# Kernel tuning notes

Hardware: AMD Instinct MI355X
Metric: run time of the kernel (lower is better)

## Reference

```python
import jax, jax.numpy as jnp
import numpy as np

N_NODES = 100_000
N_EDGES = 1_200_000
IN_C, HID_C, OUT_C, K = 64, 64, 32, 3


def setup_inputs() -> dict:
    key = jax.random.key(0)
    ks = jax.random.split(key, 8)
    x = jax.random.normal(ks[0], (N_NODES, IN_C), dtype=jnp.float32)
    edge_index = jax.random.randint(ks[1], (2, N_EDGES), 0, N_NODES, dtype=jnp.int64)
    # ChebConv parameters: weight [K, in, out], bias [out] (Glorot-ish scale)
    W1 = jax.random.normal(ks[2], (K, IN_C, HID_C), dtype=jnp.float32) / np.sqrt(IN_C)
    b1 = jnp.zeros((HID_C,), dtype=jnp.float32)
    W2 = jax.random.normal(ks[3], (K, HID_C, OUT_C), dtype=jnp.float32) / np.sqrt(HID_C)
    b2 = jnp.zeros((OUT_C,), dtype=jnp.float32)
    return {"x": x, "edge_index": edge_index, "W1": W1, "b1": b1, "W2": W2, "b2": b2}


def _cheb_conv(x, row, col, norm_w, W, b):
    # Scaled Laplacian with lambda_max=2 (PyG default): L_hat = -D^{-1/2} A D^{-1/2}
    def prop(t):  # L_hat @ t, via edge gather + segment-sum scatter
        msg = norm_w[:, None] * t[col]            # [E, C]
        return -jax.ops.segment_sum(msg, row, num_segments=N_NODES)

    Tx0 = x
    out = Tx0 @ W[0]
    Tx1 = prop(x)
    out = out + Tx1 @ W[1]
    for k in range(2, W.shape[0]):
        Tx2 = 2.0 * prop(Tx1) - Tx0          # Chebyshev recurrence
        out = out + Tx2 @ W[k]
        Tx0, Tx1 = Tx1, Tx2
    return out + b


def reference(x, edge_index, W1, b1, W2, b2):
    row, col = edge_index[0], edge_index[1]
    deg = jax.ops.segment_sum(jnp.ones((row.shape[0],), x.dtype), row,
                              num_segments=N_NODES)
    deg_inv_sqrt = jnp.where(deg > 0, jax.lax.rsqrt(jnp.maximum(deg, 1.0)), 0.0)
    norm_w = deg_inv_sqrt[row] * deg_inv_sqrt[col]   # symmetric normalization

    h = jax.nn.relu(_cheb_conv(x, row, col, norm_w, W1, b1))
    # dropout omitted (eval mode / training=False)
    return _cheb_conv(h, row, col, norm_w, W2, b2)
```

## Files before the change

### kernel.cpp

```cpp
#include <hip/hip_runtime.h>
#include <hip/hip_fp16.h>

#define N_NODES_C 100000
#define N_EDGES_C 1200000
#define NBUK ((N_NODES_C + 255) >> 8)
#define CHUNK 4096

typedef _Float16 f16x8 __attribute__((ext_vector_type(8)));
typedef float f32x4 __attribute__((ext_vector_type(4)));

__global__ __launch_bounds__(256) void hist_f2h(const int* __restrict__ ei,
                                                int* __restrict__ bucket_cnt,
                                                const float* __restrict__ x,
                                                __half* __restrict__ xh,
                                                int nedges, int n4, int histB) {
    __shared__ int cnt[NBUK];
    const int tid = threadIdx.x;
    if (blockIdx.x < histB) {
        const int base = blockIdx.x * CHUNK;
        const int nloc = min(CHUNK, nedges - base);
        for (int i = tid; i < NBUK; i += 256) cnt[i] = 0;
        __syncthreads();
        for (int i = tid; i < nloc; i += 256) atomicAdd(&cnt[ei[base + i] >> 8], 1);
        __syncthreads();
        for (int b = tid; b < NBUK; b += 256) {
            int n = cnt[b];
            if (n) atomicAdd(&bucket_cnt[b], n);
        }
    } else {
        int i = (blockIdx.x - histB) * 256 + tid;
        if (i < n4) {
            float4 v = ((const float4*)x)[i];
            __half2 tmp[2];
            tmp[0] = __floats2half2_rn(v.x, v.y);
            tmp[1] = __floats2half2_rn(v.z, v.w);
            ((float2*)xh)[i] = *(float2*)tmp;
        }
    }
}

__global__ __launch_bounds__(256) void bucket_scan(const int* __restrict__ bucket_cnt,
                                                   int* __restrict__ bucket_base,
                                                   int* __restrict__ bucket_next, int nb) {
    __shared__ int s[256];
    const int tid = threadIdx.x;
    int a0 = (2 * tid < nb) ? bucket_cnt[2 * tid] : 0;
    int a1 = (2 * tid + 1 < nb) ? bucket_cnt[2 * tid + 1] : 0;
    s[tid] = a0 + a1;
    __syncthreads();
    for (int off = 1; off < 256; off <<= 1) {
        int v = s[tid];
        int add = (tid >= off) ? s[tid - off] : 0;
        __syncthreads();
        s[tid] = v + add;
        __syncthreads();
    }
    int excl = (tid > 0) ? s[tid - 1] : 0;
    if (2 * tid < nb) { bucket_base[2 * tid] = excl; bucket_next[2 * tid] = excl; }
    if (2 * tid + 1 < nb) { bucket_base[2 * tid + 1] = excl + a0; bucket_next[2 * tid + 1] = excl + a0; }
    if (tid == 255) bucket_base[nb] = s[255];
}

__global__ __launch_bounds__(256) void bin_stage(const int* __restrict__ ei,
                                                 int* __restrict__ bucket_next,
                                                 int2* __restrict__ staged, int nedges) {
    __shared__ int cnt[NBUK];
    __shared__ int ofs[NBUK];
    __shared__ int run[NBUK];
    __shared__ int gbase[NBUK];
    __shared__ int ssum[256];
    __shared__ int2 sedge[CHUNK];
    const int tid = threadIdx.x;
    const int base = blockIdx.x * CHUNK;
    const int nloc = min(CHUNK, nedges - base);

    for (int i = tid; i < NBUK; i += 256) { cnt[i] = 0; run[i] = 0; }
    __syncthreads();

    int r[16], c[16];
#pragma unroll
    for (int k = 0; k < 16; ++k) {
        int loc = tid + k * 256;
        bool ok = loc < nloc;
        int idx = base + loc;
        r[k] = ok ? ei[idx] : -1;
        c[k] = ok ? ei[nedges + idx] : 0;
        if (ok) atomicAdd(&cnt[r[k] >> 8], 1);
    }
    __syncthreads();

    int a0 = (2 * tid < NBUK) ? cnt[2 * tid] : 0;
    int a1 = (2 * tid + 1 < NBUK) ? cnt[2 * tid + 1] : 0;
    ssum[tid] = a0 + a1;
    __syncthreads();
    for (int off = 1; off < 256; off <<= 1) {
        int v = ssum[tid];
        int add = (tid >= off) ? ssum[tid - off] : 0;
        __syncthreads();
        ssum[tid] = v + add;
        __syncthreads();
    }
    int excl = (tid > 0) ? ssum[tid - 1] : 0;
    if (2 * tid < NBUK) ofs[2 * tid] = excl;
    if (2 * tid + 1 < NBUK) ofs[2 * tid + 1] = excl + a0;
    __syncthreads();

#pragma unroll
    for (int k = 0; k < 16; ++k) {
        if (r[k] >= 0) {
            int b = r[k] >> 8;
            int p = atomicAdd(&run[b], 1);
            sedge[ofs[b] + p] = make_int2(r[k], c[k]);
        }
    }
    __syncthreads();

    for (int b = tid; b < NBUK; b += 256) {
        int n = cnt[b];
        gbase[b] = n ? atomicAdd(&bucket_next[b], n) : 0;
    }
    __syncthreads();

    for (int i = tid; i < nloc; i += 256) {
        int2 e = sedge[i];
        int b = e.x >> 8;
        staged[gbase[b] + (i - ofs[b])] = e;
    }
}

__global__ __launch_bounds__(256) void bin_count(const int2* __restrict__ staged,
                                                 const int* __restrict__ bucket_base,
                                                 int* __restrict__ rowptr, float* __restrict__ dis,
                                                 int nnodes, int nedges) {
    __shared__ int deg[256];
    __shared__ int ssum[256];
    const int b = blockIdx.x;
    const int n0 = b << 8;
    const int nend = min(n0 + 256, nnodes);
    const int nloc = nend - n0;
    const int tid = threadIdx.x;
    deg[tid] = 0;
    __syncthreads();
    const int ebase = bucket_base[b];
    const int ecount = bucket_base[b + 1] - ebase;
    for (int i = tid; i < ecount; i += 256) {
        atomicAdd(&deg[staged[ebase + i].x - n0], 1);
    }
    __syncthreads();
    int d = deg[tid];
    if (tid < nloc) {
        float df = (float)d;
        dis[n0 + tid] = (d > 0) ? (1.0f / sqrtf(fmaxf(df, 1.f))) : 0.f;
    }
    ssum[tid] = d;
    __syncthreads();
    for (int off = 1; off < 256; off <<= 1) {
        int v = ssum[tid];
        int add = (tid >= off) ? ssum[tid - off] : 0;
        __syncthreads();
        ssum[tid] = v + add;
        __syncthreads();
    }
    int excl = (tid > 0) ? ssum[tid - 1] : 0;
    if (tid < nloc) rowptr[n0 + tid] = ebase + excl;
    if (b == NBUK - 1 && tid == 0) rowptr[nnodes] = nedges;
}

__global__ __launch_bounds__(256) void bin_place(const int2* __restrict__ staged,
                                                 const int* __restrict__ rowptr,
                                                 const float* __restrict__ dis,
                                                 int2* __restrict__ colw, int nnodes) {
    __shared__ int rp[256];
    __shared__ int nx[256];
    __shared__ float dl[256];
    const int b = blockIdx.x;
    const int n0 = b << 8;
    const int nend = min(n0 + 256, nnodes);
    const int nloc = nend - n0;
    const int tid = threadIdx.x;
    if (tid < nloc) {
        rp[tid] = rowptr[n0 + tid];
        dl[tid] = dis[n0 + tid];
    }
    nx[tid] = 0;
    __syncthreads();
    const int ebase = rowptr[n0];
    const int ecount = rowptr[nend] - ebase;
    for (int i = tid; i < ecount; i += 256) {
        int2 e = staged[ebase + i];
        int rrel = e.x - n0;
        int p = atomicAdd(&nx[rrel], 1);
        float w = -dl[rrel] * dis[e.y];
        colw[rp[rrel] + p] = make_int2(e.y, __float_as_int(w));
    }
}

__global__ void fold_wf(const float* __restrict__ W1, const float* __restrict__ W2,
                        __half* __restrict__ W1f, __half* __restrict__ W2f) {
    int i = blockIdx.x * blockDim.x + threadIdx.x;
    if (i < 12288) {
        int j = i & 7;
        int lane = (i >> 3) & 63;
        int rest = i >> 9;
        int kh = rest % 6;
        int ct = rest / 6;
        int term = kh >> 1;
        int k = ((kh & 1) << 5) | ((lane >> 4) << 3) | j;
        int c = (ct << 4) | (lane & 15);
        float w0 = W1[k * 64 + c];
        float w1 = W1[4096 + k * 64 + c];
        float w2 = W1[2 * 4096 + k * 64 + c];
        float v = (term == 0) ? (w0 - w2) : ((term == 1) ? w1 : 2.0f * w2);
        W1f[i] = __float2half(v);
    } else if (i < 12288 + 6144) {
        int ii = i - 12288;
        int j = ii & 7;
        int lane = (ii >> 3) & 63;
        int rest = ii >> 9;
        int kh = rest & 1;
        int ct = rest >> 1;
        int k = (kh << 5) | ((lane >> 4) << 3) | j;
        int cg = ct * 16 + (lane & 15);
        int seg = cg >> 5;
        int c = cg & 31;
        float w0 = W2[k * 32 + c];
        float w1 = W2[2048 + k * 32 + c];
        float w2 = W2[2 * 2048 + k * 32 + c];
        float v = (seg == 0) ? (w0 - w2) : ((seg == 1) ? w1 : 2.0f * w2);
        W2f[ii] = __float2half(v);
    }
}

__global__ __launch_bounds__(256) void prop_gather_h(const __half* __restrict__ t,
                                                     const int* __restrict__ rowptr,
                                                     const int2* __restrict__ colw,
                                                     __half* __restrict__ out, int nnodes) {
    int grp = threadIdx.x >> 3;
    int ln = threadIdx.x & 7;
    int node = blockIdx.x * 32 + grp;
    if (node >= nnodes) return;
    int s = rowptr[node];
    int e = rowptr[node + 1];
    float acc[8] = {0.f, 0.f, 0.f, 0.f, 0.f, 0.f, 0.f, 0.f};
    int i = s;
    for (; i + 1 < e; i += 2) {
        int2 cw0 = colw[i];
        int2 cw1 = colw[i + 1];
        float w0 = __int_as_float(cw0.y);
        float w1 = __int_as_float(cw1.y);
        float4 r0 = ((const float4*)(t + (size_t)cw0.x * 64))[ln];
        float4 r1 = ((const float4*)(t + (size_t)cw1.x * 64))[ln];
        const __half2* h0 = (const __half2*)&r0;
        const __half2* h1 = (const __half2*)&r1;
#pragma unroll
        for (int q = 0; q < 4; ++q) {
            float2 f0 = __half22float2(h0[q]);
            float2 f1 = __half22float2(h1[q]);
            acc[2 * q + 0] += w0 * f0.x + w1 * f1.x;
            acc[2 * q + 1] += w0 * f0.y + w1 * f1.y;
        }
    }
    if (i < e) {
        int2 cw0 = colw[i];
        float w0 = __int_as_float(cw0.y);
        float4 r0 = ((const float4*)(t + (size_t)cw0.x * 64))[ln];
        const __half2* h0 = (const __half2*)&r0;
#pragma unroll
        for (int q = 0; q < 4; ++q) {
            float2 f0 = __half22float2(h0[q]);
            acc[2 * q + 0] += w0 * f0.x;
            acc[2 * q + 1] += w0 * f0.y;
        }
    }
    __half2 tmp[4];
    tmp[0] = __floats2half2_rn(acc[0], acc[1]);
    tmp[1] = __floats2half2_rn(acc[2], acc[3]);
    tmp[2] = __floats2half2_rn(acc[4], acc[5]);
    tmp[3] = __floats2half2_rn(acc[6], acc[7]);
    ((float4*)(out + (size_t)node * 64))[ln] = *(float4*)tmp;
}

template <bool F32OUT>
__global__ __launch_bounds__(256) void prop_gather32(const __half* __restrict__ t,
                                                     const int* __restrict__ rowptr,
                                                     const int2* __restrict__ colw,
                                                     const void* __restrict__ addin,
                                                     void* __restrict__ outv, int nnodes) {
    int grp = threadIdx.x >> 3;
    int ln = threadIdx.x & 7;
    int node = blockIdx.x * 32 + grp;
    if (node >= nnodes) return;
    int s = rowptr[node];
    int e = rowptr[node + 1];
    float acc[4] = {0.f, 0.f, 0.f, 0.f};
    int i = s;
    for (; i + 1 < e; i += 2) {
        int2 cw0 = colw[i];
        int2 cw1 = colw[i + 1];
        float w0 = __int_as_float(cw0.y);
        float w1 = __int_as_float(cw1.y);
        float2 r0 = ((const float2*)(t + (size_t)cw0.x * 32))[ln];
        float2 r1 = ((const float2*)(t + (size_t)cw1.x * 32))[ln];
        const __half2* h0 = (const __half2*)&r0;
        const __half2* h1 = (const __half2*)&r1;
#pragma unroll
        for (int q = 0; q < 2; ++q) {
            float2 f0 = __half22float2(h0[q]);
            float2 f1 = __half22float2(h1[q]);
            acc[2 * q + 0] += w0 * f0.x + w1 * f1.x;
            acc[2 * q + 1] += w0 * f0.y + w1 * f1.y;
        }
    }
    if (i < e) {
        int2 cw0 = colw[i];
        float w0 = __int_as_float(cw0.y);
        float2 r0 = ((const float2*)(t + (size_t)cw0.x * 32))[ln];
        const __half2* h0 = (const __half2*)&r0;
#pragma unroll
        for (int q = 0; q < 2; ++q) {
            float2 f0 = __half22float2(h0[q]);
            acc[2 * q + 0] += w0 * f0.x;
            acc[2 * q + 1] += w0 * f0.y;
        }
    }
    if (F32OUT) {
        const float* add = (const float*)addin;
        float* out = (float*)outv;
        float4 a = ((const float4*)(add + (size_t)node * 32))[ln];
        a.x += acc[0]; a.y += acc[1]; a.z += acc[2]; a.w += acc[3];
        ((float4*)(out + (size_t)node * 32))[ln] = a;
    } else {
        const __half* add = (const __half*)addin;
        __half* out = (__half*)outv;
        float2 raw = ((const float2*)(add + (size_t)node * 32))[ln];
        const __half2* hp = (const __half2*)&raw;
        float2 a0 = __half22float2(hp[0]);
        float2 a1 = __half22float2(hp[1]);
        __half2 tmp[2];
        tmp[0] = __floats2half2_rn(acc[0] + a0.x, acc[1] + a0.y);
        tmp[1] = __floats2half2_rn(acc[2] + a1.x, acc[3] + a1.y);
        ((float2*)(out + (size_t)node * 32))[ln] = *(float2*)tmp;
    }
}

__global__ __launch_bounds__(256) void gemm_fused(const __half* __restrict__ A0,
                                                  const __half* __restrict__ A1,
                                                  const __half* __restrict__ A2,
                                                  const __half* __restrict__ W1f,
                                                  const float* __restrict__ b1,
                                                  const __half* __restrict__ W2f,
                                                  const float* __restrict__ b2,
                                                  float* __restrict__ P0,
                                                  __half* __restrict__ G1,
                                                  __half* __restrict__ G2, int nnodes) {
    __shared__ __align__(16) __half htile[4][16 * 72];
    const int wave = threadIdx.x >> 6;
    const int lane = threadIdx.x & 63;
    const int node0 = blockIdx.x * 64 + wave * 16;
    const int m = lane & 15;
    const int quad = lane >> 4;
    int arow = node0 + m;
    if (arow >= nnodes) arow = nnodes - 1;

    const __half* Ap[3] = {A0, A1, A2};
    f16x8 a[6];
#pragma unroll
    for (int kh = 0; kh < 6; ++kh) {
        const __half* A = Ap[kh >> 1];
        a[kh] = *(const f16x8*)(A + (size_t)arow * 64 + ((kh & 1) << 5) + (quad << 3));
    }
    __half* ht = htile[wave];
#pragma unroll
    for (int ct = 0; ct < 4; ++ct) {
        f32x4 acc = {0.f, 0.f, 0.f, 0.f};
#pragma unroll
        for (int kh = 0; kh < 6; ++kh) {
            f16x8 b = *(const f16x8*)(W1f + ((size_t)(ct * 6 + kh) * 64 + lane) * 8);
            acc = __builtin_amdgcn_mfma_f32_16x16x32_f16(a[kh], b, acc, 0, 0, 0);
        }
        int col = (ct << 4) | m;
        float bias = b1[col];
#pragma unroll
        for (int r = 0; r < 4; ++r) {
            ht[(quad * 4 + r) * 72 + col] = __float2half(fmaxf(acc[r] + bias, 0.f));
        }
    }
    __syncthreads();

    f16x8 h0 = *(const f16x8*)(ht + m * 72 + (quad << 3));
    f16x8 h1 = *(const f16x8*)(ht + m * 72 + 32 + (quad << 3));
#pragma unroll
    for (int ct = 0; ct < 6; ++ct) {
        f32x4 acc = {0.f, 0.f, 0.f, 0.f};
        f16x8 b0 = *(const f16x8*)(W2f + ((size_t)(ct * 2 + 0) * 64 + lane) * 8);
        f16x8 b1v = *(const f16x8*)(W2f + ((size_t)(ct * 2 + 1) * 64 + lane) * 8);
        acc = __builtin_amdgcn_mfma_f32_16x16x32_f16(h0, b0, acc, 0, 0, 0);
        acc = __builtin_amdgcn_mfma_f32_16x16x32_f16(h1, b1v, acc, 0, 0, 0);
        int seg = ct >> 1;
        int c = ((ct & 1) << 4) | m;
#pragma unroll
        for (int r = 0; r < 4; ++r) {
            int n = node0 + (quad << 2) + r;
            if (n >= nnodes) continue;
            float v = acc[r];
            if (seg == 0)      P0[(size_t)n * 32 + c] = v + b2[c];
            else if (seg == 1) G1[(size_t)n * 32 + c] = __float2half(v);
            else               G2[(size_t)n * 32 + c] = __float2half(v);
        }
    }
}

extern "C" void kernel_launch(void* const* d_in, const int* in_sizes, int n_in,
                              void* d_out, int out_size, void* d_ws, size_t ws_size,
                              hipStream_t stream) {
    const float* x  = (const float*)d_in[0];
    const int*   ei = (const int*)d_in[1];
    const float* W1 = (const float*)d_in[2];
    const float* b1 = (const float*)d_in[3];
    const float* W2 = (const float*)d_in[4];
    const float* b2 = (const float*)d_in[5];
    float* out = (float*)d_out;

    const int NN = N_NODES_C;
    const int NE = N_EDGES_C;
    const size_t HFEAT_BYTES = (size_t)NN * 64 * sizeof(__half);
    const size_t H32_BYTES = (size_t)NN * 32 * sizeof(__half);

    char* ws = (char*)d_ws;
    size_t off = 0;
    auto alloc = [&](size_t bytes) -> void* {
        void* p = ws + off;
        off += (bytes + 255) & ~(size_t)255;
        return p;
    };
    int*    bucket_cnt  = (int*)alloc((size_t)NBUK * 4);
    int*    bucket_base = (int*)alloc((size_t)(NBUK + 1) * 4);
    int*    bucket_next = (int*)alloc((size_t)NBUK * 4);
    int*    rowptr      = (int*)alloc((size_t)(NN + 1) * 4);
    float*  dis         = (float*)alloc((size_t)NN * 4);
    int2*   staged      = (int2*)alloc((size_t)NE * 8);
    int2*   colw        = (int2*)alloc((size_t)NE * 8);
    __half* xh          = (__half*)alloc(HFEAT_BYTES);
    __half* T1h         = (__half*)alloc(HFEAT_BYTES);
    __half* T2h         = (__half*)alloc(HFEAT_BYTES);
    __half* Qh          = (__half*)alloc(H32_BYTES);
    float*  P0          = (float*)alloc((size_t)NN * 32 * 4);
    __half* W1f         = (__half*)alloc((size_t)4 * 6 * 64 * 8 * 2);
    __half* W2f         = (__half*)alloc((size_t)6 * 2 * 64 * 8 * 2);

    const int PROPB = (NN + 31) / 32;
    const int CONV4 = NN * 64 / 4;
    const int CONVB = (CONV4 + 255) / 256;
    const int BINB = (NE + CHUNK - 1) / CHUNK;
    const int GEMMB = (NN + 63) / 64;

    hipMemsetAsync(bucket_cnt, 0, (size_t)NBUK * 4, stream);
    hist_f2h<<<BINB + CONVB, 256, 0, stream>>>(ei, bucket_cnt, x, xh, NE, CONV4, BINB);
    bucket_scan<<<1, 256, 0, stream>>>(bucket_cnt, bucket_base, bucket_next, NBUK);
    bin_stage<<<BINB, 256, 0, stream>>>(ei, bucket_next, staged, NE);
    bin_count<<<NBUK, 256, 0, stream>>>(staged, bucket_base, rowptr, dis, NN, NE);
    bin_place<<<NBUK, 256, 0, stream>>>(staged, rowptr, dis, colw, NN);
    fold_wf<<<(18432 + 255) / 256, 256, 0, stream>>>(W1, W2, W1f, W2f);

    prop_gather_h<<<PROPB, 256, 0, stream>>>(xh, rowptr, colw, T1h, NN);
    prop_gather_h<<<PROPB, 256, 0, stream>>>(T1h, rowptr, colw, T2h, NN);
    gemm_fused<<<GEMMB, 256, 0, stream>>>(xh, T1h, T2h, W1f, b1, W2f, b2, P0, T1h, T2h, NN);

    prop_gather32<false><<<PROPB, 256, 0, stream>>>(T2h, rowptr, colw, T1h, Qh, NN);
    prop_gather32<true><<<PROPB, 256, 0, stream>>>(Qh, rowptr, colw, P0, out, NN);
}
```

Measured before the change: 256.1 us.

## Pack staged edges into 32-bit, merge scan with weight fold, unroll gathers by four

The staged edge buffer now stores each edge as one 32-bit word, with the column in the low 17 bits and the row offset within its bucket in the high bits. This halves the staging write and read traffic. The bucket scan and the weight-fold kernels are merged into one launch to save a launch. Both gather kernels are unrolled from two to four edges per iteration so more independent row loads are in flight, at the cost of more registers.

```diff
diff --git a/kernel.cpp b/kernel.cpp
--- a/kernel.cpp
+++ b/kernel.cpp
@@ -8,6 +8,10 @@
 
 typedef _Float16 f16x8 __attribute__((ext_vector_type(8)));
 typedef float f32x4 __attribute__((ext_vector_type(4)));
+
+#define PACK(r8, c) ((c) | ((r8) << 17))
+#define UNPACK_C(v) ((v) & 0x1FFFF)
+#define UNPACK_R(v) ((v) >> 17)
 
 __global__ __launch_bounds__(256) void hist_f2h(const int* __restrict__ ei,
                                                 int* __restrict__ bucket_cnt,
@@ -39,165 +43,34 @@
     }
 }
 
-__global__ __launch_bounds__(256) void bucket_scan(const int* __restrict__ bucket_cnt,
-                                                   int* __restrict__ bucket_base,
-                                                   int* __restrict__ bucket_next, int nb) {
-    __shared__ int s[256];
+__global__ __launch_bounds__(256) void scan_fold(const int* __restrict__ bucket_cnt,
+                                                 int* __restrict__ bucket_base,
+                                                 int* __restrict__ bucket_next, int nb,
+                                                 const float* __restrict__ W1,
+                                                 const float* __restrict__ W2,
+                                                 __half* __restrict__ W1f,
+                                                 __half* __restrict__ W2f) {
     const int tid = threadIdx.x;
-    int a0 = (2 * tid < nb) ? bucket_cnt[2 * tid] : 0;
-    int a1 = (2 * tid + 1 < nb) ? bucket_cnt[2 * tid + 1] : 0;
-    s[tid] = a0 + a1;
-    __syncthreads();
-    for (int off = 1; off < 256; off <<= 1) {
-        int v = s[tid];
-        int add = (tid >= off) ? s[tid - off] : 0;
-        __syncthreads();
-        s[tid] = v + add;
-        __syncthreads();
-    }
-    int excl = (tid > 0) ? s[tid - 1] : 0;
-    if (2 * tid < nb) { bucket_base[2 * tid] = excl; bucket_next[2 * tid] = excl; }
-    if (2 * tid + 1 < nb) { bucket_base[2 * tid + 1] = excl + a0; bucket_next[2 * tid + 1] = excl + a0; }
-    if (tid == 255) bucket_base[nb] = s[255];
-}
-
-__global__ __launch_bounds__(256) void bin_stage(const int* __restrict__ ei,
-                                                 int* __restrict__ bucket_next,
-                                                 int2* __restrict__ staged, int nedges) {
-    __shared__ int cnt[NBUK];
-    __shared__ int ofs[NBUK];
-    __shared__ int run[NBUK];
-    __shared__ int gbase[NBUK];
-    __shared__ int ssum[256];
-    __shared__ int2 sedge[CHUNK];
-    const int tid = threadIdx.x;
-    const int base = blockIdx.x * CHUNK;
-    const int nloc = min(CHUNK, nedges - base);
-
-    for (int i = tid; i < NBUK; i += 256) { cnt[i] = 0; run[i] = 0; }
-    __syncthreads();
-
-    int r[16], c[16];
-#pragma unroll
-    for (int k = 0; k < 16; ++k) {
-        int loc = tid + k * 256;
-        bool ok = loc < nloc;
-        int idx = base + loc;
-        r[k] = ok ? ei[idx] : -1;
-        c[k] = ok ? ei[nedges + idx] : 0;
-        if (ok) atomicAdd(&cnt[r[k] >> 8], 1);
-    }
-    __syncthreads();
-
-    int a0 = (2 * tid < NBUK) ? cnt[2 * tid] : 0;
-    int a1 = (2 * tid + 1 < NBUK) ? cnt[2 * tid + 1] : 0;
-    ssum[tid] = a0 + a1;
-    __syncthreads();
-    for (int off = 1; off < 256; off <<= 1) {
-        int v = ssum[tid];
-        int add = (tid >= off) ? ssum[tid - off] : 0;
-        __syncthreads();
-        ssum[tid] = v + add;
-        __syncthreads();
-    }
-    int excl = (tid > 0) ? ssum[tid - 1] : 0;
-    if (2 * tid < NBUK) ofs[2 * tid] = excl;
-    if (2 * tid + 1 < NBUK) ofs[2 * tid + 1] = excl + a0;
-    __syncthreads();
-
-#pragma unroll
-    for (int k = 0; k < 16; ++k) {
-        if (r[k] >= 0) {
-            int b = r[k] >> 8;
-            int p = atomicAdd(&run[b], 1);
-            sedge[ofs[b] + p] = make_int2(r[k], c[k]);
-        }
-    }
-    __syncthreads();
-
-    for (int b = tid; b < NBUK; b += 256) {
-        int n = cnt[b];
-        gbase[b] = n ? atomicAdd(&bucket_next[b], n) : 0;
-    }
-    __syncthreads();
-
-    for (int i = tid; i < nloc; i += 256) {
-        int2 e = sedge[i];
-        int b = e.x >> 8;
-        staged[gbase[b] + (i - ofs[b])] = e;
-    }
-}
-
-__global__ __launch_bounds__(256) void bin_count(const int2* __restrict__ staged,
-                                                 const int* __restrict__ bucket_base,
-                                                 int* __restrict__ rowptr, float* __restrict__ dis,
-                                                 int nnodes, int nedges) {
-    __shared__ int deg[256];
-    __shared__ int ssum[256];
-    const int b = blockIdx.x;
-    const int n0 = b << 8;
-    const int nend = min(n0 + 256, nnodes);
-    const int nloc = nend - n0;
-    const int tid = threadIdx.x;
-    deg[tid] = 0;
-    __syncthreads();
-    const int ebase = bucket_base[b];
-    const int ecount = bucket_base[b + 1] - ebase;
-    for (int i = tid; i < ecount; i += 256) {
-        atomicAdd(&deg[staged[ebase + i].x - n0], 1);
-    }
-    __syncthreads();
-    int d = deg[tid];
-    if (tid < nloc) {
-        float df = (float)d;
-        dis[n0 + tid] = (d > 0) ? (1.0f / sqrtf(fmaxf(df, 1.f))) : 0.f;
-    }
-    ssum[tid] = d;
-    __syncthreads();
-    for (int off = 1; off < 256; off <<= 1) {
-        int v = ssum[tid];
-        int add = (tid >= off) ? ssum[tid - off] : 0;
-        __syncthreads();
-        ssum[tid] = v + add;
-        __syncthreads();
-    }
-    int excl = (tid > 0) ? ssum[tid - 1] : 0;
-    if (tid < nloc) rowptr[n0 + tid] = ebase + excl;
-    if (b == NBUK - 1 && tid == 0) rowptr[nnodes] = nedges;
-}
-
-__global__ __launch_bounds__(256) void bin_place(const int2* __restrict__ staged,
-                                                 const int* __restrict__ rowptr,
-                                                 const float* __restrict__ dis,
-                                                 int2* __restrict__ colw, int nnodes) {
-    __shared__ int rp[256];
-    __shared__ int nx[256];
-    __shared__ float dl[256];
-    const int b = blockIdx.x;
-    const int n0 = b << 8;
-    const int nend = min(n0 + 256, nnodes);
-    const int nloc = nend - n0;
-    const int tid = threadIdx.x;
-    if (tid < nloc) {
-        rp[tid] = rowptr[n0 + tid];
-        dl[tid] = dis[n0 + tid];
-    }
-    nx[tid] = 0;
-    __syncthreads();
-    const int ebase = rowptr[n0];
-    const int ecount = rowptr[nend] - ebase;
-    for (int i = tid; i < ecount; i += 256) {
-        int2 e = staged[ebase + i];
-        int rrel = e.x - n0;
-        int p = atomicAdd(&nx[rrel], 1);
-        float w = -dl[rrel] * dis[e.y];
-        colw[rp[rrel] + p] = make_int2(e.y, __float_as_int(w));
-    }
-}
-
-__global__ void fold_wf(const float* __restrict__ W1, const float* __restrict__ W2,
-                        __half* __restrict__ W1f, __half* __restrict__ W2f) {
-    int i = blockIdx.x * blockDim.x + threadIdx.x;
+    if (blockIdx.x == 0) {
+        __shared__ int s[256];
+        int a0 = (2 * tid < nb) ? bucket_cnt[2 * tid] : 0;
+        int a1 = (2 * tid + 1 < nb) ? bucket_cnt[2 * tid + 1] : 0;
+        s[tid] = a0 + a1;
+        __syncthreads();
+        for (int off = 1; off < 256; off <<= 1) {
+            int v = s[tid];
+            int add = (tid >= off) ? s[tid - off] : 0;
+            __syncthreads();
+            s[tid] = v + add;
+            __syncthreads();
+        }
+        int excl = (tid > 0) ? s[tid - 1] : 0;
+        if (2 * tid < nb) { bucket_base[2 * tid] = excl; bucket_next[2 * tid] = excl; }
+        if (2 * tid + 1 < nb) { bucket_base[2 * tid + 1] = excl + a0; bucket_next[2 * tid + 1] = excl + a0; }
+        if (tid == 255) bucket_base[nb] = s[255];
+        return;
+    }
+    int i = (blockIdx.x - 1) * 256 + tid;
     if (i < 12288) {
         int j = i & 7;
         int lane = (i >> 3) & 63;
@@ -231,6 +104,141 @@
     }
 }
 
+__global__ __launch_bounds__(256) void bin_stage(const int* __restrict__ ei,
+                                                 int* __restrict__ bucket_next,
+                                                 int* __restrict__ staged, int nedges) {
+    __shared__ int cnt[NBUK];
+    __shared__ int ofs[NBUK];
+    __shared__ int run[NBUK];
+    __shared__ int gbase[NBUK];
+    __shared__ int ssum[256];
+    __shared__ int2 sedge[CHUNK];
+    const int tid = threadIdx.x;
+    const int base = blockIdx.x * CHUNK;
+    const int nloc = min(CHUNK, nedges - base);
+
+    for (int i = tid; i < NBUK; i += 256) { cnt[i] = 0; run[i] = 0; }
+    __syncthreads();
+
+    int r[16], c[16];
+#pragma unroll
+    for (int k = 0; k < 16; ++k) {
+        int loc = tid + k * 256;
+        bool ok = loc < nloc;
+        int idx = base + loc;
+        r[k] = ok ? ei[idx] : -1;
+        c[k] = ok ? ei[nedges + idx] : 0;
+        if (ok) atomicAdd(&cnt[r[k] >> 8], 1);
+    }
+    __syncthreads();
+
+    int a0 = (2 * tid < NBUK) ? cnt[2 * tid] : 0;
+    int a1 = (2 * tid + 1 < NBUK) ? cnt[2 * tid + 1] : 0;
+    ssum[tid] = a0 + a1;
+    __syncthreads();
+    for (int off = 1; off < 256; off <<= 1) {
+        int v = ssum[tid];
+        int add = (tid >= off) ? ssum[tid - off] : 0;
+        __syncthreads();
+        ssum[tid] = v + add;
+        __syncthreads();
+    }
+    int excl = (tid > 0) ? ssum[tid - 1] : 0;
+    if (2 * tid < NBUK) ofs[2 * tid] = excl;
+    if (2 * tid + 1 < NBUK) ofs[2 * tid + 1] = excl + a0;
+    __syncthreads();
+
+#pragma unroll
+    for (int k = 0; k < 16; ++k) {
+        if (r[k] >= 0) {
+            int b = r[k] >> 8;
+            int p = atomicAdd(&run[b], 1);
+            sedge[ofs[b] + p] = make_int2(r[k], c[k]);
+        }
+    }
+    __syncthreads();
+
+    for (int b = tid; b < NBUK; b += 256) {
+        int n = cnt[b];
+        gbase[b] = n ? atomicAdd(&bucket_next[b], n) : 0;
+    }
+    __syncthreads();
+
+    for (int i = tid; i < nloc; i += 256) {
+        int2 e = sedge[i];
+        int b = e.x >> 8;
+        staged[gbase[b] + (i - ofs[b])] = PACK(e.x & 255, e.y);
+    }
+}
+
+__global__ __launch_bounds__(256) void bin_count(const int* __restrict__ staged,
+                                                 const int* __restrict__ bucket_base,
+                                                 int* __restrict__ rowptr, float* __restrict__ dis,
+                                                 int nnodes, int nedges) {
+    __shared__ int deg[256];
+    __shared__ int ssum[256];
+    const int b = blockIdx.x;
+    const int n0 = b << 8;
+    const int nend = min(n0 + 256, nnodes);
+    const int nloc = nend - n0;
+    const int tid = threadIdx.x;
+    deg[tid] = 0;
+    __syncthreads();
+    const int ebase = bucket_base[b];
+    const int ecount = bucket_base[b + 1] - ebase;
+    for (int i = tid; i < ecount; i += 256) {
+        atomicAdd(&deg[UNPACK_R(staged[ebase + i])], 1);
+    }
+    __syncthreads();
+    int d = deg[tid];
+    if (tid < nloc) {
+        float df = (float)d;
+        dis[n0 + tid] = (d > 0) ? (1.0f / sqrtf(fmaxf(df, 1.f))) : 0.f;
+    }
+    ssum[tid] = d;
+    __syncthreads();
+    for (int off = 1; off < 256; off <<= 1) {
+        int v = ssum[tid];
+        int add = (tid >= off) ? ssum[tid - off] : 0;
+        __syncthreads();
+        ssum[tid] = v + add;
+        __syncthreads();
+    }
+    int excl = (tid > 0) ? ssum[tid - 1] : 0;
+    if (tid < nloc) rowptr[n0 + tid] = ebase + excl;
+    if (b == NBUK - 1 && tid == 0) rowptr[nnodes] = nedges;
+}
+
+__global__ __launch_bounds__(256) void bin_place(const int* __restrict__ staged,
+                                                 const int* __restrict__ rowptr,
+                                                 const float* __restrict__ dis,
+                                                 int2* __restrict__ colw, int nnodes) {
+    __shared__ int rp[256];
+    __shared__ int nx[256];
+    __shared__ float dl[256];
+    const int b = blockIdx.x;
+    const int n0 = b << 8;
+    const int nend = min(n0 + 256, nnodes);
+    const int nloc = nend - n0;
+    const int tid = threadIdx.x;
+    if (tid < nloc) {
+        rp[tid] = rowptr[n0 + tid];
+        dl[tid] = dis[n0 + tid];
+    }
+    nx[tid] = 0;
+    __syncthreads();
+    const int ebase = rowptr[n0];
+    const int ecount = rowptr[nend] - ebase;
+    for (int i = tid; i < ecount; i += 256) {
+        int v = staged[ebase + i];
+        int col = UNPACK_C(v);
+        int rrel = UNPACK_R(v);
+        int p = atomicAdd(&nx[rrel], 1);
+        float w = -dl[rrel] * dis[col];
+        colw[rp[rrel] + p] = make_int2(col, __float_as_int(w));
+    }
+}
+
 __global__ __launch_bounds__(256) void prop_gather_h(const __half* __restrict__ t,
                                                      const int* __restrict__ rowptr,
                                                      const int2* __restrict__ colw,
@@ -243,24 +251,34 @@
     int e = rowptr[node + 1];
     float acc[8] = {0.f, 0.f, 0.f, 0.f, 0.f, 0.f, 0.f, 0.f};
     int i = s;
-    for (; i + 1 < e; i += 2) {
+    for (; i + 3 < e; i += 4) {
         int2 cw0 = colw[i];
         int2 cw1 = colw[i + 1];
+        int2 cw2 = colw[i + 2];
+        int2 cw3 = colw[i + 3];
+        float4 r0 = ((const float4*)(t + (size_t)cw0.x * 64))[ln];
+        float4 r1 = ((const float4*)(t + (size_t)cw1.x * 64))[ln];
+        float4 r2 = ((const float4*)(t + (size_t)cw2.x * 64))[ln];
+        float4 r3 = ((const float4*)(t + (size_t)cw3.x * 64))[ln];
         float w0 = __int_as_float(cw0.y);
         float w1 = __int_as_float(cw1.y);
-        float4 r0 = ((const float4*)(t + (size_t)cw0.x * 64))[ln];
-        float4 r1 = ((const float4*)(t + (size_t)cw1.x * 64))[ln];
+        float w2 = __int_as_float(cw2.y);
+        float w3 = __int_as_float(cw3.y);
         const __half2* h0 = (const __half2*)&r0;
         const __half2* h1 = (const __half2*)&r1;
+        const __half2* h2 = (const __half2*)&r2;
+        const __half2* h3 = (const __half2*)&r3;
 #pragma unroll
         for (int q = 0; q < 4; ++q) {
             float2 f0 = __half22float2(h0[q]);
             float2 f1 = __half22float2(h1[q]);
-            acc[2 * q + 0] += w0 * f0.x + w1 * f1.x;
-            acc[2 * q + 1] += w0 * f0.y + w1 * f1.y;
-        }
-    }
-    if (i < e) {
+            float2 f2 = __half22float2(h2[q]);
+            float2 f3 = __half22float2(h3[q]);
+            acc[2 * q + 0] += w0 * f0.x + w1 * f1.x + w2 * f2.x + w3 * f3.x;
+            acc[2 * q + 1] += w0 * f0.y + w1 * f1.y + w2 * f2.y + w3 * f3.y;
+        }
+    }
+    for (; i < e; ++i) {
         int2 cw0 = colw[i];
         float w0 = __int_as_float(cw0.y);
         float4 r0 = ((const float4*)(t + (size_t)cw0.x * 64))[ln];
@@ -294,24 +312,34 @@
     int e = rowptr[node + 1];
     float acc[4] = {0.f, 0.f, 0.f, 0.f};
     int i = s;
-    for (; i + 1 < e; i += 2) {
+    for (; i + 3 < e; i += 4) {
         int2 cw0 = colw[i];
         int2 cw1 = colw[i + 1];
+        int2 cw2 = colw[i + 2];
+        int2 cw3 = colw[i + 3];
+        float2 r0 = ((const float2*)(t + (size_t)cw0.x * 32))[ln];
+        float2 r1 = ((const float2*)(t + (size_t)cw1.x * 32))[ln];
+        float2 r2 = ((const float2*)(t + (size_t)cw2.x * 32))[ln];
+        float2 r3 = ((const float2*)(t + (size_t)cw3.x * 32))[ln];
         float w0 = __int_as_float(cw0.y);
         float w1 = __int_as_float(cw1.y);
-        float2 r0 = ((const float2*)(t + (size_t)cw0.x * 32))[ln];
-        float2 r1 = ((const float2*)(t + (size_t)cw1.x * 32))[ln];
+        float w2 = __int_as_float(cw2.y);
+        float w3 = __int_as_float(cw3.y);
         const __half2* h0 = (const __half2*)&r0;
         const __half2* h1 = (const __half2*)&r1;
+        const __half2* h2 = (const __half2*)&r2;
+        const __half2* h3 = (const __half2*)&r3;
 #pragma unroll
         for (int q = 0; q < 2; ++q) {
             float2 f0 = __half22float2(h0[q]);
             float2 f1 = __half22float2(h1[q]);
-            acc[2 * q + 0] += w0 * f0.x + w1 * f1.x;
-            acc[2 * q + 1] += w0 * f0.y + w1 * f1.y;
-        }
-    }
-    if (i < e) {
+            float2 f2 = __half22float2(h2[q]);
+            float2 f3 = __half22float2(h3[q]);
+            acc[2 * q + 0] += w0 * f0.x + w1 * f1.x + w2 * f2.x + w3 * f3.x;
+            acc[2 * q + 1] += w0 * f0.y + w1 * f1.y + w2 * f2.y + w3 * f3.y;
+        }
+    }
+    for (; i < e; ++i) {
         int2 cw0 = colw[i];
         float w0 = __int_as_float(cw0.y);
         float2 r0 = ((const float2*)(t + (size_t)cw0.x * 32))[ln];
@@ -438,7 +466,7 @@
     int*    bucket_next = (int*)alloc((size_t)NBUK * 4);
     int*    rowptr      = (int*)alloc((size_t)(NN + 1) * 4);
     float*  dis         = (float*)alloc((size_t)NN * 4);
-    int2*   staged      = (int2*)alloc((size_t)NE * 8);
+    int*    staged      = (int*)alloc((size_t)NE * 4);
     int2*   colw        = (int2*)alloc((size_t)NE * 8);
     __half* xh          = (__half*)alloc(HFEAT_BYTES);
     __half* T1h         = (__half*)alloc(HFEAT_BYTES);
@@ -453,14 +481,15 @@
     const int CONVB = (CONV4 + 255) / 256;
     const int BINB = (NE + CHUNK - 1) / CHUNK;
     const int GEMMB = (NN + 63) / 64;
+    const int FOLDB = 1 + (18432 + 255) / 256;
 
     hipMemsetAsync(bucket_cnt, 0, (size_t)NBUK * 4, stream);
     hist_f2h<<<BINB + CONVB, 256, 0, stream>>>(ei, bucket_cnt, x, xh, NE, CONV4, BINB);
-    bucket_scan<<<1, 256, 0, stream>>>(bucket_cnt, bucket_base, bucket_next, NBUK);
+    scan_fold<<<FOLDB, 256, 0, stream>>>(bucket_cnt, bucket_base, bucket_next, NBUK,
+                                         W1, W2, W1f, W2f);
     bin_stage<<<BINB, 256, 0, stream>>>(ei, bucket_next, staged, NE);
     bin_count<<<NBUK, 256, 0, stream>>>(staged, bucket_base, rowptr, dis, NN, NE);
     bin_place<<<NBUK, 256, 0, stream>>>(staged, rowptr, dis, colw, NN);
-    fold_wf<<<(18432 + 255) / 256, 256, 0, stream>>>(W1, W2, W1f, W2f);
 
     prop_gather_h<<<PROPB, 256, 0, stream>>>(xh, rowptr, colw, T1h, NN);
     prop_gather_h<<<PROPB, 256, 0, stream>>>(T1h, rowptr, colw, T2h, NN);
```

Measured after the change: 245.0 us. 1.05x faster.
